# Optimization experiments

Measured on AMD Instinct MI355X. Metric: run time of the kernel, lower is better.

The kernel has to match this reference:

```python
import jax, jax.numpy as jnp
import numpy as np

B, T, D = 16, 2048, 512
DB, K, TOPK, WIN = 128, 7, 16, 64
GATE_CAP = 0.5
STRAND_CAP = 0.5
_PHI = 1.618033988749895
_PSI = -0.6180339887498949


def _ln(x, w, b):
    mu = jnp.mean(x, -1, keepdims=True)
    var = jnp.var(x, -1, keepdims=True)
    return (x - mu) * jax.lax.rsqrt(var + 1e-5) * w + b


def setup_inputs() -> dict:
    key = jax.random.key(0)
    ks = jax.random.split(key, 20)
    def nrm(i, shape, scale=1.0):
        return jax.random.normal(ks[i], shape, dtype=jnp.float32) * jnp.float32(scale)
    return {
        'X_write': nrm(0, (B, T, D)),
        'X_read': nrm(1, (B, T, D)),
        'slots': nrm(2, (B, K, DB)),
        'W0': nrm(3, (D, D), D ** -0.5),
        'ln_write_w': jnp.ones((D,), jnp.float32),
        'ln_write_b': jnp.zeros((D,), jnp.float32),
        'W_V': nrm(4, (D, DB), D ** -0.5),
        'W_K_slot': nrm(5, (DB, DB), DB ** -0.5),
        'slot_key_bias': nrm(6, (K, DB), 2.0),
        'W_gate_w': nrm(7, (2 * DB, DB), (2 * DB) ** -0.5),
        'W_gate_b': jnp.full((DB,), -2.0, jnp.float32),
        'ln_strand_w': jnp.ones((DB,), jnp.float32),
        'ln_strand_b': jnp.zeros((DB,), jnp.float32),
        'Ws_Q': nrm(8, (DB, DB), DB ** -0.5),
        'Ws_K': nrm(9, (DB, DB), DB ** -0.5),
        'Ws_V': nrm(10, (DB, DB), DB ** -0.5),
        'lambda_strand': nrm(11, (DB,), 0.5),
        'W_Q_read': nrm(12, (D, DB), D ** -0.5),
        'W_K_read': nrm(13, (DB, DB), DB ** -0.5),
        'W_V_read': nrm(14, (DB, D), DB ** -0.5),
        'render_coeffs': nrm(15, (K, 3, D), 0.2),
        'slot_temps': jnp.ones((K,), jnp.float32),
    }


def _forward(X_write, X_read, slots, W0, ln_write_w, ln_write_b, W_V, W_K_slot,
             slot_key_bias, W_gate_w, W_gate_b, ln_strand_w, ln_strand_b,
             Ws_Q, Ws_K, Ws_V, lambda_strand, W_Q_read, W_K_read, W_V_read,
             render_coeffs, slot_temps):
    scale = jnp.float32(DB ** -0.5)
    W0_sg = jax.lax.stop_gradient(W0)
    X_n = _ln(X_write, ln_write_w, ln_write_b)

    # ---- windowed salience + topk pair selection (no-grad in original) ----
    X_nsg = jax.lax.stop_gradient(X_n)
    X_W0 = X_nsg @ W0_sg.T                      # [B,T,D]
    NEG = jnp.float32(-1e30)
    sal = []
    for o in range(1, WIN + 1):                 # offset j = i - o, fixed small loop
        s = jnp.sum(X_nsg[:, o:, :] * X_W0[:, :-o, :], axis=-1)  # [B, T-o]
        sal.append(jnp.pad(s, ((0, 0), (o, 0)), constant_values=NEG))
    sal = jnp.stack(sal, axis=-1).reshape(B, T * WIN)
    _, flat_idx = jax.lax.top_k(sal, TOPK)      # [B, TOPK]
    i_idx = flat_idx // WIN
    j_idx = i_idx - (flat_idx % WIN + 1)

    # ---- gather pairs, salience-weighted relation vector ----
    x_newer = jnp.take_along_axis(X_n, i_idx[:, :, None], axis=1)   # [B,TOPK,D]
    x_older = jnp.take_along_axis(X_n, j_idx[:, :, None], axis=1)
    pair_sal = jnp.sum(x_newer * (x_older @ W0_sg.T), axis=-1)      # [B,TOPK]
    alpha = jax.nn.softmax(pair_sal, axis=-1)
    rel = (x_newer - x_older) @ W_V                                 # [B,TOPK,DB]
    R_t = jnp.einsum('bk,bkd->bd', alpha, rel)                      # [B,DB]

    # ---- gated slot write ----
    slot_keys = slots @ W_K_slot + slot_key_bias                    # [B,K,DB]
    compat = jnp.einsum('bkd,bd->bk', slot_keys, R_t) * scale * jax.nn.softplus(slot_temps)
    sw = jax.nn.softmax(compat, axis=-1)
    weighted_R = sw[:, :, None] * R_t[:, None, :]                   # [B,K,DB]
    g = jax.nn.sigmoid(jnp.concatenate([slots, weighted_R], -1) @ W_gate_w + W_gate_b)
    slots_upd = (1.0 - g) * slots + g * weighted_R

    # ---- K x K strand mixer ----
    Bn = _ln(slots_upd, ln_strand_w, ln_strand_b)
    sa = jax.nn.softmax(jnp.einsum('bqd,bkd->bqk', Bn @ Ws_Q, Bn @ Ws_K) * scale, axis=-1)
    ctx = sa @ (Bn @ Ws_V)
    slots_next = slots_upd + ctx * jnp.clip(jnp.tanh(lambda_strand), -STRAND_CAP, STRAND_CAP)

    # ---- aux losses ----
    L_persist = jnp.mean((slots_next - slots) ** 2)
    nrm = jnp.maximum(jnp.linalg.norm(slots_next, axis=-1, keepdims=True), 1e-12)
    Bnorm = slots_next / nrm
    cos = jnp.einsum('bkd,bjd->bkj', Bnorm, Bnorm)
    off = ~jnp.eye(K, dtype=bool)
    L_div = jnp.mean((cos ** 2)[:, off])

    # ---- directional gated read attention ----
    q_r = X_read @ W_Q_read                                         # [B,T,DB]
    k_r = slots_next @ W_K_read                                     # [B,K,DB]
    v_r = slots_next @ W_V_read                                     # [B,K,D]
    scores = jnp.einsum('btd,bkd->btk', q_r, k_r) * scale
    q_mean = jnp.mean(X_read, axis=1)                               # [B,D]
    w0q = q_mean @ W0_sg.T
    denom = jnp.float32(_PHI - _PSI)
    phi_q = (w0q - _PSI * q_mean) / denom
    psi_q = (_PHI * q_mean - w0q) / denom
    phi_mag = jnp.linalg.norm(phi_q, axis=-1, keepdims=True)
    psi_mag = jnp.linalg.norm(psi_q, axis=-1, keepdims=True)
    total = phi_mag + psi_mag + 1e-6
    basis = jnp.concatenate([jnp.ones_like(phi_mag), phi_mag / total, psi_mag / total], -1)  # [B,3]
    gate = jnp.clip(jnp.tanh(jnp.einsum('bi,kid->bkd', basis, render_coeffs)), -GATE_CAP, GATE_CAP)
    z = jnp.einsum('btk,bkd->btd', jax.nn.softmax(scores, axis=-1), v_r * gate)
    return z, slots_next, L_persist, L_div


def reference(X_write, X_read, slots, W0, ln_write_w, ln_write_b, W_V, W_K_slot,
              slot_key_bias, W_gate_w, W_gate_b, ln_strand_w, ln_strand_b,
              Ws_Q, Ws_K, Ws_V, lambda_strand, W_Q_read, W_K_read, W_V_read,
              render_coeffs, slot_temps):
    return _forward(X_write, X_read, slots, W0, ln_write_w, ln_write_b, W_V, W_K_slot,
                    slot_key_bias, W_gate_w, W_gate_b, ln_strand_w, ln_strand_b,
                    Ws_Q, Ws_K, Ws_V, lambda_strand, W_Q_read, W_K_read, W_V_read,
                    render_coeffs, slot_temps)
```

## Files before the change

kernel.cpp:

```cpp
#include <hip/hip_runtime.h>
#include <math.h>

#define B_ 16
#define T_ 2048
#define D_ 512
#define DB_ 128
#define K_ 7
#define TOPK_ 16
#define WIN_ 64

static constexpr float SCALE_ = 0.08838834764831845f;
static constexpr float PHI_ = 1.618033988749895f;
static constexpr float PSI_ = -0.6180339887498949f;
static constexpr float INV_DENOM_ = 0.4472135954999579f;
static constexpr float NEGV = -1e30f;
static constexpr float NEGINF = -3.402823466e38f;
#define IMAXI 0x7FFFFFFF

typedef __attribute__((ext_vector_type(8))) __bf16 bf16x8;
typedef __attribute__((ext_vector_type(8))) unsigned short u16x8;
typedef __attribute__((ext_vector_type(4))) float f32x4;

__device__ inline float softplusf(float x){
    return fmaxf(x, 0.f) + log1pf(expf(-fabsf(x)));
// ... 99 lines not shown
        qpart[((size_t)b_*32 + c)*D_ + tid] = s0;
        qpart[((size_t)b_*32 + c)*D_ + tid + 256] = s1;
    }
}

__global__ __launch_bounds__(256) void gemm_xw0_mfma(const unsigned short* __restrict__ Ah,
                                                     const unsigned short* __restrict__ Al,
                                                     const unsigned short* __restrict__ Wh,
                                                     const unsigned short* __restrict__ Wl,
                                                     float* __restrict__ Cf)
{
    __shared__ __align__(16) unsigned short sAh[2*128*32], sAl[2*128*32], sBh[2*128*32], sBl[2*128*32];
    int t0 = blockIdx.x * 128, d0 = blockIdx.y * 128;
    int tid = threadIdx.x;
    int lane = tid & 63, wid = tid >> 6;
    int wr = wid >> 1, wc = wid & 1;
    int fr = lane & 15;
    int kc2 = ((((lane >> 4) + (fr >> 1)) & 3) * 8);

    f32x4 acc[4][4];
    #pragma unroll
    for (int m = 0; m < 4; m++)
        #pragma unroll
        for (int n = 0; n < 4; n++) acc[m][n] = (f32x4){0.f,0.f,0.f,0.f};

    const unsigned short* gs = (wid==0) ? Ah : (wid==1) ? Al : (wid==2) ? Wh : Wl;
    unsigned short* lsA = (wid==0) ? sAh : (wid==1) ? sAl : (wid==2) ? sBh : sBl;
    int rowoff = (wid < 2) ? t0 : d0;
    int cch = ((lane & 3) - ((lane >> 3) & 3)) & 3;
    const unsigned short* gbase = gs + (size_t)(rowoff + (lane >> 2))*512 + cch*8;

    #pragma unroll
    for (int i = 0; i < 8; i++)
        gload16(gbase + (size_t)(16*i)*512 + 0, lsA + i*512);

    for (int t = 0; t < 16; t++) {
        int cur = t & 1;
        __syncthreads();
        if (t < 15) {
            unsigned short* ls = lsA + (cur^1)*(128*32);
            int kk = (t+1)*32;
            #pragma unroll
            for (int i = 0; i < 8; i++)
                gload16(gbase + (size_t)(16*i)*512 + kk, ls + i*512);
        }
        int bo = cur*(128*32);
        bf16x8 ahf[4], alf[4], bhf[4], blf[4];
        #pragma unroll
        for (int m = 0; m < 4; m++) {
            int r = bo + (wr*64 + m*16 + fr)*32 + kc2;
            ahf[m] = ld_bf8(&sAh[r]);
            alf[m] = ld_bf8(&sAl[r]);
        }
        #pragma unroll
        for (int n = 0; n < 4; n++) {
            int r = bo + (wc*64 + n*16 + fr)*32 + kc2;
            bhf[n] = ld_bf8(&sBh[r]);
            blf[n] = ld_bf8(&sBl[r]);
        }
        #pragma unroll
        for (int m = 0; m < 4; m++)
            #pragma unroll
            for (int n = 0; n < 4; n++) {
                acc[m][n] = __builtin_amdgcn_mfma_f32_16x16x32_bf16(bhf[n], ahf[m], acc[m][n], 0, 0, 0);
                acc[m][n] = __builtin_amdgcn_mfma_f32_16x16x32_bf16(bhf[n], alf[m], acc[m][n], 0, 0, 0);
                acc[m][n] = __builtin_amdgcn_mfma_f32_16x16x32_bf16(blf[n], ahf[m], acc[m][n], 0, 0, 0);
            }
    }

    #pragma unroll
    for (int m = 0; m < 4; m++) {
        int t = t0 + wr*64 + m*16 + fr;
        #pragma unroll
        for (int n = 0; n < 4; n++) {
            int dbase = d0 + wc*64 + n*16 + (lane >> 4)*4;
            *(f32x4*)&Cf[(size_t)t*512 + dbase] = acc[m][n];
        }
    }
}

__global__ __launch_bounds__(256) void sal_mfma(const unsigned short* __restrict__ Xh,
                                                const unsigned short* __restrict__ Xl,
                                                const float* __restrict__ Cf,
                                                float* __restrict__ sal)
{
    int b = blockIdx.x, i0 = blockIdx.y * 64;
    __shared__ __align__(16) unsigned short sAh[64*32], sAl[64*32], sBh[128*32], sBl[128*32];
    int tid = threadIdx.x;
    int lane = tid & 63, wcw = tid >> 6;
    int fr = lane & 15;
    int kc2 = ((((lane >> 4) + (fr >> 1)) & 3) * 8);

    const unsigned short* XhB = Xh + (size_t)b*T_*D_;
    const unsigned short* XlB = Xl + (size_t)b*T_*D_;
    const float* CfB = Cf + (size_t)b*T_*D_;

    f32x4 acc[4][2];
    #pragma unroll
    for (int m = 0; m < 4; m++) { acc[m][0] = (f32x4){0.f,0.f,0.f,0.f}; acc[m][1] = (f32x4){0.f,0.f,0.f,0.f}; }

    int ar = tid >> 2, ac = tid & 3;
    int aslot = (ac + (ar >> 1)) & 3;
    int brow = tid >> 1, bhh = tid & 1;
    int jrow = i0 - 64 + brow;

    uint4 rAh, rAl;
    float4 rB0[2], rB1[2];

    auto LOAD = [&](int kk){
        rAh = *(const uint4*)(XhB + (size_t)(i0 + ar)*512 + kk + ac*8);
        rAl = *(const uint4*)(XlB + (size_t)(i0 + ar)*512 + kk + ac*8);
        #pragma unroll
        for (int cc = 0; cc < 2; cc++) {
            int c = 2*bhh + cc;
            if (jrow >= 0) {
                const float* src = CfB + (size_t)jrow*512 + kk + c*8;
                rB0[cc] = *(const float4*)src;
                rB1[cc] = *(const float4*)(src + 4);
            } else {
                rB0[cc] = make_float4(0.f,0.f,0.f,0.f);
                rB1[cc] = make_float4(0.f,0.f,0.f,0.f);
            }
        }
    };
    auto WRITE = [&](){
        *(uint4*)&sAh[ar*32 + aslot*8] = rAh;
        *(uint4*)&sAl[ar*32 + aslot*8] = rAl;
        #pragma unroll
        for (int cc = 0; cc < 2; cc++) {
            int c = 2*bhh + cc;
            int slot = (c + (brow >> 1)) & 3;
            uint4 hv, lv;
            float4 v0 = rB0[cc], v1 = rB1[cc];
            unsigned int h01 = pkbf(v0.x, v0.y), h23 = pkbf(v0.z, v0.w);
            unsigned int h45 = pkbf(v1.x, v1.y), h67 = pkbf(v1.z, v1.w);
            float r0 = v0.x - __uint_as_float(h01 << 16);
            float r1 = v0.y - __uint_as_float(h01 & 0xFFFF0000u);
            float r2 = v0.z - __uint_as_float(h23 << 16);
            float r3 = v0.w - __uint_as_float(h23 & 0xFFFF0000u);
            float r4 = v1.x - __uint_as_float(h45 << 16);
            float r5 = v1.y - __uint_as_float(h45 & 0xFFFF0000u);
            float r6 = v1.z - __uint_as_float(h67 << 16);
            float r7 = v1.w - __uint_as_float(h67 & 0xFFFF0000u);
            hv.x = h01; hv.y = h23; hv.z = h45; hv.w = h67;
            lv.x = pkbf(r0, r1); lv.y = pkbf(r2, r3); lv.z = pkbf(r4, r5); lv.w = pkbf(r6, r7);
            *(uint4*)&sBh[brow*32 + slot*8] = hv;
            *(uint4*)&sBl[brow*32 + slot*8] = lv;
        }
    };

    LOAD(0);
    for (int t = 0; t < 16; t++) {
        WRITE();
        __syncthreads();
        int kkn = (t+1)*32;
        bf16x8 ahf[4], alf[4], bhf[2], blf[2];
        #pragma unroll
        for (int m = 0; m < 4; m++) {
            int r = (m*16 + fr)*32 + kc2;
            ahf[m] = ld_bf8(&sAh[r]);
            alf[m] = ld_bf8(&sAl[r]);
        }
        #pragma unroll
        for (int n = 0; n < 2; n++) {
            int r = (wcw*32 + n*16 + fr)*32 + kc2;
            bhf[n] = ld_bf8(&sBh[r]);
            blf[n] = ld_bf8(&sBl[r]);
        }
        if (t < 15) LOAD(kkn);
        #pragma unroll
        for (int m = 0; m < 4; m++)
            #pragma unroll
            for (int n = 0; n < 2; n++) {
                acc[m][n] = __builtin_amdgcn_mfma_f32_16x16x32_bf16(ahf[m], bhf[n], acc[m][n], 0, 0, 0);
                acc[m][n] = __builtin_amdgcn_mfma_f32_16x16x32_bf16(ahf[m], blf[n], acc[m][n], 0, 0, 0);
                acc[m][n] = __builtin_amdgcn_mfma_f32_16x16x32_bf16(alf[m], bhf[n], acc[m][n], 0, 0, 0);
            }
        __syncthreads();
    }

    float* salB = sal + (size_t)b*T_*WIN_;
    #pragma unroll
    for (int m = 0; m < 4; m++) {
        #pragma unroll
        for (int n = 0; n < 2; n++) {
            int jl = wcw*32 + n*16 + fr;
            #pragma unroll
            for (int r = 0; r < 4; r++) {
                int il = m*16 + (lane >> 4)*4 + r;
                int o = il - jl + 64;
                if (o >= 1 && o <= 64) {
                    int jg = i0 - 64 + jl;
                    salB[(size_t)(i0 + il)*WIN_ + (o - 1)] = (jg >= 0) ? acc[m][n][r] : NEGV;
                }
            }
        }
    }
}

__global__ __launch_bounds__(256) void topk_stage1(const float* __restrict__ sal,
                                                   float* __restrict__ cv, int* __restrict__ ci,
                                                   const float* __restrict__ qpart,
                                                   const float* __restrict__ W0,
                                                   float* __restrict__ w0p)
{
    int b = blockIdx.x, tid = threadIdx.x;
    if (blockIdx.y >= 64) {
        int c = blockIdx.y - 64;
        __shared__ float qm[D_];
        for (int p = tid; p < D_; p += 256) {
            float s = 0.f;
            for (int cc = 0; cc < 32; cc++) s += qpart[((size_t)b*32 + cc)*D_ + p];
            qm[p] = s * (1.f/2048.f);
        }
        __syncthreads();
        int w = tid >> 6, lane = tid & 63;
        float ph = 0.f, ps = 0.f;
        for (int r = 0; r < 16; r++) {
            int d = c*64 + w*16 + r;
            const float* wr = W0 + (size_t)d*D_;
            float s = 0.f;
            #pragma unroll
            for (int q = 0; q < 8; q++) s += qm[lane + q*64] * wr[lane + q*64];
            #pragma unroll
            for (int off = 32; off; off >>= 1) s += __shfl_xor(s, off);
            float phi = (s - PSI_*qm[d]) * INV_DENOM_;
            float psi = (PHI_*qm[d] - s) * INV_DENOM_;
            ph += phi*phi; ps += psi*psi;
        }
        __shared__ float shp[4], shs[4];
        if (lane == 0) { shp[w] = ph; shs[w] = ps; }
        __syncthreads();
        if (tid == 0) {
            w0p[((size_t)b*8 + c)*2 + 0] = shp[0]+shp[1]+shp[2]+shp[3];
            w0p[((size_t)b*8 + c)*2 + 1] = shs[0]+shs[1]+shs[2]+shs[3];
        }
        return;
    }
    int c = blockIdx.y;
    const float* s = sal + (size_t)b*(T_*WIN_) + (size_t)c*2048;
    int base = c*2048;
    int lane = tid & 63, wvi = tid >> 6;
    float v0=NEGINF,v1=NEGINF,v2=NEGINF,v3=NEGINF,v4=NEGINF,v5=NEGINF,v6=NEGINF,v7=NEGINF;
    int   i0=IMAXI, i1=IMAXI, i2=IMAXI, i3=IMAXI, i4=IMAXI, i5=IMAXI, i6=IMAXI, i7=IMAXI;
    #pragma unroll
    for (int r = 0; r < 8; r++) {
        int p = tid + r*256;
        float v = s[p];
        int idx = base + p;
        if (v > v7 || (v == v7 && idx < i7)) {
            bool b6 = (v > v6) || (v == v6 && idx < i6);
            bool b5 = (v > v5) || (v == v5 && idx < i5);
            bool b4 = (v > v4) || (v == v4 && idx < i4);
            bool b3 = (v > v3) || (v == v3 && idx < i3);
            bool b2 = (v > v2) || (v == v2 && idx < i2);
            bool b1 = (v > v1) || (v == v1 && idx < i1);
            bool b0 = (v > v0) || (v == v0 && idx < i0);
            float n7 = b6 ? v6 : v;             int m7 = b6 ? i6 : idx;
            float n6 = b6 ? (b5 ? v5 : v) : v6; int m6 = b6 ? (b5 ? i5 : idx) : i6;
            float n5 = b5 ? (b4 ? v4 : v) : v5; int m5 = b5 ? (b4 ? i4 : idx) : i5;
            float n4 = b4 ? (b3 ? v3 : v) : v4; int m4 = b4 ? (b3 ? i3 : idx) : i4;
            float n3 = b3 ? (b2 ? v2 : v) : v3; int m3 = b3 ? (b2 ? i2 : idx) : i3;
            float n2 = b2 ? (b1 ? v1 : v) : v2; int m2 = b2 ? (b1 ? i1 : idx) : i2;
            float n1 = b1 ? (b0 ? v0 : v) : v1; int m1 = b1 ? (b0 ? i0 : idx) : i1;
            float n0 = b0 ? v : v0;             int m0 = b0 ? idx : i0;
            v7=n7;i7=m7; v6=n6;i6=m6; v5=n5;i5=m5; v4=n4;i4=m4;
            v3=n3;i3=m3; v2=n2;i2=m2; v1=n1;i1=m1; v0=n0;i0=m0;
        }
    }
    float* cvo = cv + (((size_t)b*64 + c)*64) + wvi*16;
    int*   cio = ci + (((size_t)b*64 + c)*64) + wvi*16;
    for (int r = 0; r < 16; r++) {
        float bv = v0; int bi = i0;
        float wv_ = bv; int wi = bi;
        #pragma unroll
        for (int off = 1; off < 64; off <<= 1) {
            float vx = __shfl_xor(wv_, off);
            int   ix = __shfl_xor(wi, off);
            if (vx > wv_ || (vx == wv_ && ix < wi)) { wv_ = vx; wi = ix; }
        }
        if (bv == wv_ && bi == wi) {
            v0=v1;i0=i1; v1=v2;i1=i2; v2=v3;i2=i3; v3=v4;i3=i4;
            v4=v5;i4=i5; v5=v6;i5=i6; v6=v7;i6=i7; v7=NEGINF;i7=IMAXI;
        }
        if (lane == 0) { cvo[r] = wv_; cio[r] = wi; }
    }
}

__global__ __launch_bounds__(512) void slot_head(
    const unsigned short* __restrict__ Xh, const unsigned short* __restrict__ Xl,
    const float* __restrict__ cv, const int* __restrict__ ci,
    float* __restrict__ yws)
{
    int b = blockIdx.x, tid = threadIdx.x;
    int lane = tid & 63, wvi = tid >> 6;
    __shared__ float scv[128]; __shared__ int sci[128];
    __shared__ float tvv[16]; __shared__ int tii[16];
    __shared__ float alpha[16]; __shared__ int tis[16], tjs[16];

    const float* cvb = cv + (size_t)b*4096;
    const int*   cib = ci + (size_t)b*4096;
    float v0=NEGINF,v1=NEGINF,v2=NEGINF,v3=NEGINF,v4=NEGINF,v5=NEGINF,v6=NEGINF,v7=NEGINF;
    int   i0=IMAXI, i1=IMAXI, i2=IMAXI, i3=IMAXI, i4=IMAXI, i5=IMAXI, i6=IMAXI, i7=IMAXI;
    #pragma unroll
    for (int r = 0; r < 8; r++) {
        int p = tid + r*512;
        float v = cvb[p];
        int idx = cib[p];
        if (v > v7 || (v == v7 && idx < i7)) {
            bool b6 = (v > v6) || (v == v6 && idx < i6);
            bool b5 = (v > v5) || (v == v5 && idx < i5);
            bool b4 = (v > v4) || (v == v4 && idx < i4);
            bool b3 = (v > v3) || (v == v3 && idx < i3);
            bool b2 = (v > v2) || (v == v2 && idx < i2);
            bool b1 = (v > v1) || (v == v1 && idx < i1);
            bool b0 = (v > v0) || (v == v0 && idx < i0);
            float n7 = b6 ? v6 : v;             int m7 = b6 ? i6 : idx;
            float n6 = b6 ? (b5 ? v5 : v) : v6; int m6 = b6 ? (b5 ? i5 : idx) : i6;
            float n5 = b5 ? (b4 ? v4 : v) : v5; int m5 = b5 ? (b4 ? i4 : idx) : i5;
            float n4 = b4 ? (b3 ? v3 : v) : v4; int m4 = b4 ? (b3 ? i3 : idx) : i4;
            float n3 = b3 ? (b2 ? v2 : v) : v3; int m3 = b3 ? (b2 ? i2 : idx) : i3;
            float n2 = b2 ? (b1 ? v1 : v) : v2; int m2 = b2 ? (b1 ? i1 : idx) : i2;
            float n1 = b1 ? (b0 ? v0 : v) : v1; int m1 = b1 ? (b0 ? i0 : idx) : i1;
            float n0 = b0 ? v : v0;             int m0 = b0 ? idx : i0;
            v7=n7;i7=m7; v6=n6;i6=m6; v5=n5;i5=m5; v4=n4;i4=m4;
            v3=n3;i3=m3; v2=n2;i2=m2; v1=n1;i1=m1; v0=n0;i0=m0;
        }
    }
    for (int r = 0; r < 16; r++) {
        float bv = v0; int bi = i0;
        float wv_ = bv; int wi = bi;
        #pragma unroll
        for (int off = 1; off < 64; off <<= 1) {
            float vx = __shfl_xor(wv_, off);
            int   ix = __shfl_xor(wi, off);
            if (vx > wv_ || (vx == wv_ && ix < wi)) { wv_ = vx; wi = ix; }
        }
        if (bv == wv_ && bi == wi) {
            v0=v1;i0=i1; v1=v2;i1=i2; v2=v3;i2=i3; v3=v4;i3=i4;
            v4=v5;i4=i5; v5=v6;i5=i6; v6=v7;i6=i7; v7=NEGINF;i7=IMAXI;
        }
        if (lane == 0) { scv[wvi*16 + r] = wv_; sci[wvi*16 + r] = wi; }
    }
    __syncthreads();
    if (wvi == 0) {
        float a0 = scv[lane], a1 = scv[lane + 64];
        int   e0 = sci[lane], e1 = sci[lane + 64];
        bool sw = (a1 > a0) || (a1 == a0 && e1 < e0);
        float u0 = sw ? a1 : a0; int j0 = sw ? e1 : e0;
        float u1 = sw ? a0 : a1; int j1 = sw ? e0 : e1;
        for (int r = 0; r < 16; r++) {
            float bv = u0; int bi = j0;
            float wv_ = bv; int wi = bi;
            #pragma unroll
            for (int off = 1; off < 64; off <<= 1) {
                float vx = __shfl_xor(wv_, off);
                int   ix = __shfl_xor(wi, off);
                if (vx > wv_ || (vx == wv_ && ix < wi)) { wv_ = vx; wi = ix; }
            }
            if (bv == wv_ && bi == wi) { u0 = u1; j0 = j1; u1 = NEGINF; j1 = IMAXI; }
            if (lane == 0) { tvv[r] = wv_; tii[r] = wi; }
        }
    }
    __syncthreads();
    if (tid < 16) {
        float v = tvv[tid];
        int flat = tii[tid];
        tis[tid] = flat >> 6;
        tjs[tid] = (flat >> 6) - ((flat & 63) + 1);
        float m = v;
        #pragma unroll
        for (int off = 8; off; off >>= 1) m = fmaxf(m, __shfl_xor(m, off, 16));
        float e = expf(v - m);
        float s = e;
        #pragma unroll
        for (int off = 8; off; off >>= 1) s += __shfl_xor(s, off, 16);
        alpha[tid] = e / s;
    }
    __syncthreads();
    {
        float acc = 0.f;
        #pragma unroll
        for (int k = 0; k < 16; k++) {
            int i = tis[k], j = tjs[k];
            float xi = bf2f(Xh[((size_t)b*T_ + i)*D_ + tid]) + bf2f(Xl[((size_t)b*T_ + i)*D_ + tid]);
            float xj = bf2f(Xh[((size_t)b*T_ + j)*D_ + tid]) + bf2f(Xl[((size_t)b*T_ + j)*D_ + tid]);
            acc += alpha[k] * (xi - xj);
        }
        yws[(size_t)b*D_ + tid] = acc;
    }
}

__global__ __launch_bounds__(256) void slot_rt(const float* __restrict__ yws,
                                               const float* __restrict__ W_V,
                                               float* __restrict__ rtp)
{
    int b = blockIdx.x, c = blockIdx.y, tid = threadIdx.x;
    __shared__ float ysl[64];
    __shared__ float hsum[2][DB_];
    if (tid < 64) ysl[tid] = yws[(size_t)b*D_ + c*64 + tid];
    __syncthreads();
    int d = tid & 127, h = tid >> 7;
    float acc = 0.f;
    int e0 = h*32;
    #pragma unroll 8
    for (int e = e0; e < e0 + 32; e++)
        acc += ysl[e] * W_V[(size_t)(c*64 + e)*DB_ + d];
    hsum[h][d] = acc;
    __syncthreads();
    if (tid < DB_) rtp[((size_t)b*8 + c)*DB_ + tid] = hsum[0][tid] + hsum[1][tid];
}

__global__ __launch_bounds__(1024) void slot_main(
    const float* __restrict__ slots_in, const float* __restrict__ rtp,
    const float* __restrict__ W_K_slot, const float* __restrict__ skb,
    const float* __restrict__ Wg, const float* __restrict__ Wgb,
    const float* __restrict__ lnw, const float* __restrict__ lnb,
    const float* __restrict__ WsQ, const float* __restrict__ WsK, const float* __restrict__ WsV,
    const float* __restrict__ lambda_, const float* __restrict__ temps,
    float* __restrict__ snws, float* __restrict__ out_slots,
    float* __restrict__ lpP, float* __restrict__ lpD)
{
    int b = blockIdx.x, tid = threadIdx.x;
    int lane = tid & 63, wvi = tid >> 6;
    __shared__ __align__(16) float wbuf[2*8192];
    __shared__ float Rt[DB_];
    __shared__ float sl[K_][DB_];
    __shared__ float upd[K_][DB_];
    __shared__ float Bn[K_][DB_];
    __shared__ float qq[K_][DB_], kk2[K_][DB_], vv[K_][DB_];
    __shared__ float snsh[K_][DB_];
    __shared__ float pf[1024];
    __shared__ float swv[K_], compat[K_], mu7[K_], rs7[K_], nr7[K_], ldv[K_];
    __shared__ float sa[K_][K_];

    auto ISSUE = [&](const float* src, int buf){
        const float* g = src + (wvi*2)*256 + lane*4;
        float* l = wbuf + buf*8192 + (wvi*2)*256;
        gload16(g, l);
        gload16(g + 256, l + 256);
    };

    int kk_ = tid >> 7, dd_ = tid & 127;
    bool act = tid < K_*DB_;

    ISSUE(W_K_slot, 0);
    for (int p = tid; p < K_*DB_; p += 1024) sl[p>>7][p&127] = slots_in[(size_t)b*K_*DB_ + p];
    if (tid < DB_) {
        float a = 0.f;
        #pragma unroll
        for (int c = 0; c < 8; c++) a += rtp[((size_t)b*8 + c)*DB_ + tid];
        Rt[tid] = a;
    }
    __syncthreads();
    ISSUE(W_K_slot + 8192, 1);
    float kacc = 0.f;
    if (act) {
        #pragma unroll 8
        for (int e = 0; e < 64; e++) kacc += sl[kk_][e] * wbuf[e*DB_ + dd_];
    }
    __syncthreads();
    ISSUE(Wg, 0);
    if (act) {
        #pragma unroll 8
        for (int e = 0; e < 64; e++) kacc += sl[kk_][64+e] * wbuf[8192 + e*DB_ + dd_];
        qq[kk_][dd_] = (kacc + skb[kk_*DB_ + dd_]) * Rt[dd_];
    }
    __syncthreads();
    if (wvi < K_) {
        float acc = qq[wvi][lane] + qq[wvi][lane + 64];
        #pragma unroll
        for (int off = 32; off; off >>= 1) acc += __shfl_xor(acc, off);
        if (lane == 0) compat[wvi] = acc * SCALE_ * softplusf(temps[wvi]);
    }
    __syncthreads();
    if (tid == 0) {
        float m = compat[0];
        for (int k = 1; k < K_; k++) m = fmaxf(m, compat[k]);
        float ssum = 0.f;
        for (int k = 0; k < K_; k++) { float e = expf(compat[k]-m); swv[k] = e; ssum += e; }
        for (int k = 0; k < K_; k++) swv[k] /= ssum;
    }
    __syncthreads();
    ISSUE(Wg + 8192, 1);
    float gacc = 0.f;
    if (act) {
        #pragma unroll 8
        for (int e = 0; e < 64; e++) gacc += sl[kk_][e] * wbuf[e*DB_ + dd_];
    }
    __syncthreads();
    ISSUE(Wg + 16384, 0);
    if (act) {
        #pragma unroll 8
        for (int e = 0; e < 64; e++) gacc += sl[kk_][64+e] * wbuf[8192 + e*DB_ + dd_];
    }
    __syncthreads();
    ISSUE(Wg + 24576, 1);
    float g2acc = 0.f;
    if (act) {
        #pragma unroll 8
        for (int e = 0; e < 64; e++) g2acc += Rt[e] * wbuf[e*DB_ + dd_];
    }
    __syncthreads();
    ISSUE(WsQ, 0);
    if (act) {
        #pragma unroll 8
        for (int e = 0; e < 64; e++) g2acc += Rt[64+e] * wbuf[8192 + e*DB_ + dd_];
        float pre = gacc + swv[kk_]*g2acc + Wgb[dd_];
        float g = 1.f / (1.f + expf(-pre));
        upd[kk_][dd_] = (1.f - g) * sl[kk_][dd_] + g * (swv[kk_] * Rt[dd_]);
    }
    __syncthreads();
    if (wvi < K_) {
        float a0 = upd[wvi][lane], a1 = upd[wvi][lane + 64];
        float s = a0 + a1, ss = a0*a0 + a1*a1;
        #pragma unroll
        for (int off = 32; off; off >>= 1) { s += __shfl_xor(s, off); ss += __shfl_xor(ss, off); }
        if (lane == 0) {
            float mu = s / (float)DB_;
            mu7[wvi] = mu;
            rs7[wvi] = rsqrtf(ss/(float)DB_ - mu*mu + 1e-5f);
        }
    }
    __syncthreads();
    if (act) Bn[kk_][dd_] = (upd[kk_][dd_] - mu7[kk_]) * rs7[kk_] * lnw[dd_] + lnb[dd_];
    __syncthreads();
    ISSUE(WsQ + 8192, 1);
    float qacc = 0.f;
    if (act) {
        #pragma unroll 8
        for (int e = 0; e < 64; e++) qacc += Bn[kk_][e] * wbuf[e*DB_ + dd_];
    }
    __syncthreads();
    ISSUE(WsK, 0);
    if (act) {
        #pragma unroll 8
        for (int e = 0; e < 64; e++) qacc += Bn[kk_][64+e] * wbuf[8192 + e*DB_ + dd_];
// ... 166 lines not shown
    __shared__ float vgs[K_][D_];
    int tid = threadIdx.x;
    for (int p = tid; p < K_*D_; p += 256) {
        kqs[p>>9][p&511] = kq[(size_t)b*K_*D_ + p];
        vgs[p>>9][p&511] = vg[(size_t)b*K_*D_ + p];
    }
    __syncthreads();
    int lane = tid & 63, w = tid >> 6;
    for (int it = 0; it < 16; it++) {
        int t = t0 + w*16 + it;
        const float* x = Xr + ((size_t)b*T_ + t)*D_;
        float xr[8];
        float s[K_] = {0,0,0,0,0,0,0};
        #pragma unroll
        for (int r = 0; r < 8; r++) {
            int e = lane + r*64;
            xr[r] = x[e];
            #pragma unroll
            for (int k = 0; k < K_; k++) s[k] += xr[r] * kqs[k][e];
        }
        #pragma unroll
        for (int k = 0; k < K_; k++)
            for (int off = 32; off; off >>= 1) s[k] += __shfl_xor(s[k], off);
        float sc[K_];
        float m = NEGINF;
        #pragma unroll
        for (int k = 0; k < K_; k++) { sc[k] = s[k] * SCALE_; m = fmaxf(m, sc[k]); }
        float p[K_], ssum = 0.f;
        #pragma unroll
        for (int k = 0; k < K_; k++) { p[k] = expf(sc[k] - m); ssum += p[k]; }
        float inv = 1.f / ssum;
        float* zp = z + ((size_t)b*T_ + t)*D_;
        #pragma unroll
        for (int r = 0; r < 8; r++) {
            int e = lane + r*64;
            float a = 0.f;
            #pragma unroll
            for (int k = 0; k < K_; k++) a += p[k] * vgs[k][e];
            zp[e] = a * inv;
        }
    }
}

extern "C" void kernel_launch(void* const* d_in, const int* in_sizes, int n_in,
                              void* d_out, int out_size, void* d_ws, size_t ws_size,
                              hipStream_t stream)
{
    const float* X_write = (const float*)d_in[0];
    const float* X_read  = (const float*)d_in[1];
    const float* slots   = (const float*)d_in[2];
    const float* W0      = (const float*)d_in[3];
    const float* lnw_w   = (const float*)d_in[4];
    const float* lnw_b   = (const float*)d_in[5];
    const float* W_V     = (const float*)d_in[6];
    const float* W_K_slot= (const float*)d_in[7];
    const float* skb     = (const float*)d_in[8];
    const float* Wg      = (const float*)d_in[9];
    const float* Wgb     = (const float*)d_in[10];
    const float* lns_w   = (const float*)d_in[11];
    const float* lns_b   = (const float*)d_in[12];
    const float* WsQ     = (const float*)d_in[13];
    const float* WsK     = (const float*)d_in[14];
    const float* WsV     = (const float*)d_in[15];
    const float* lambda_ = (const float*)d_in[16];
    const float* WQr     = (const float*)d_in[17];
    const float* WKr     = (const float*)d_in[18];
    const float* WVr     = (const float*)d_in[19];
    const float* rc      = (const float*)d_in[20];
    const float* temps   = (const float*)d_in[21];

    const size_t NXD = (size_t)B_*T_*D_;
    unsigned short* Xh  = (unsigned short*)d_ws;
    unsigned short* Xl  = Xh + NXD;
    float* Cf           = (float*)(Xl + NXD);
    unsigned short* W0h = (unsigned short*)(Cf + NXD);
    unsigned short* W0l = W0h + (size_t)D_*D_;
    float* fscr  = (float*)(W0l + (size_t)D_*D_);
    float* qpart = fscr;
    float* w0p   = qpart + (size_t)B_*32*D_;
    float* snws  = w0p + 256;
    float* kq    = snws + (size_t)B_*K_*DB_;
    float* vg    = kq + (size_t)B_*K_*D_;
    float* cv    = vg + (size_t)B_*K_*D_;
    int*   ci    = (int*)(cv + (size_t)B_*64*64);
    float* lpP   = (float*)(ci + (size_t)B_*64*64);
    float* lpD   = lpP + 16;
    float* yws   = lpD + 16;
    float* rtp   = yws + (size_t)B_*D_;

    float* z_out     = (float*)d_out;
    float* slots_out = z_out + NXD;
    float* loss_out  = slots_out + (size_t)B_*K_*DB_;
    float* sal       = z_out;

    prep_kernel<<<dim3(4096 + 256 + 512), dim3(256), 0, stream>>>(
        X_write, lnw_w, lnw_b, Xh, Xl, W0, W0h, W0l, X_read, qpart);
    gemm_xw0_mfma<<<dim3(B_*T_/128, D_/128), dim3(256), 0, stream>>>(Xh, Xl, W0h, W0l, Cf);
    sal_mfma<<<dim3(B_, T_/64), dim3(256), 0, stream>>>(Xh, Xl, Cf, sal);
    topk_stage1<<<dim3(B_, 72), dim3(256), 0, stream>>>(sal, cv, ci, qpart, W0, w0p);
    slot_head<<<dim3(B_), dim3(512), 0, stream>>>(Xh, Xl, cv, ci, yws);
    slot_rt<<<dim3(B_, 8), dim3(256), 0, stream>>>(yws, W_V, rtp);
    slot_main<<<dim3(B_), dim3(1024), 0, stream>>>(slots, rtp,
        W_K_slot, skb, Wg, Wgb, lns_w, lns_b, WsQ, WsK, WsV, lambda_, temps,
        snws, slots_out, lpP, lpD);
    kqvg_kernel<<<dim3(B_, K_), dim3(256), 0, stream>>>(snws, WKr, WQr, WVr, rc, w0p,
        lpP, lpD, kq, vg, loss_out);
    z_kernel<<<dim3(B_, T_/64), dim3(256), 0, stream>>>(X_read, kq, vg, z_out);
}
```

Baseline: 265.5 us.

## Fuse salience top-k into sal_mfma and merge slot_head/slot_rt into slot_main

The salience tile now stays in shared memory and sal_mfma computes per-row-chunk top-16 candidates directly, so the full salience array is no longer written to global memory and reread by a separate top-k kernel. The final candidate merge, the pair gather and the W_V projection move into slot_main, with W_V streamed through its double buffer, which removes two small launches and their intermediates. The W0·q path becomes its own small kernel. In exchange sal_mfma uses more shared memory (16 KB extra), and the single-block-per-batch slot_main takes on more serial work.

```diff
diff --git a/kernel.cpp b/kernel.cpp
--- a/kernel.cpp
+++ b/kernel.cpp
@@ -205,10 +205,11 @@
 __global__ __launch_bounds__(256) void sal_mfma(const unsigned short* __restrict__ Xh,
                                                 const unsigned short* __restrict__ Xl,
                                                 const float* __restrict__ Cf,
-                                                float* __restrict__ sal)
+                                                float* __restrict__ cv, int* __restrict__ ci)
 {
     int b = blockIdx.x, i0 = blockIdx.y * 64;
     __shared__ __align__(16) unsigned short sAh[64*32], sAl[64*32], sBh[128*32], sBl[128*32];
+    __shared__ float stile[64*64];
     int tid = threadIdx.x;
     int lane = tid & 63, wcw = tid >> 6;
     int fr = lane & 15;
@@ -302,7 +303,6 @@
         __syncthreads();
     }
 
-    float* salB = sal + (size_t)b*T_*WIN_;
     #pragma unroll
     for (int m = 0; m < 4; m++) {
         #pragma unroll
@@ -314,166 +314,47 @@
                 int o = il - jl + 64;
                 if (o >= 1 && o <= 64) {
                     int jg = i0 - 64 + jl;
-                    salB[(size_t)(i0 + il)*WIN_ + (o - 1)] = (jg >= 0) ? acc[m][n][r] : NEGV;
+                    stile[il*64 + (o - 1)] = (jg >= 0) ? acc[m][n][r] : NEGV;
                 }
             }
         }
     }
-}
-
-__global__ __launch_bounds__(256) void topk_stage1(const float* __restrict__ sal,
-                                                   float* __restrict__ cv, int* __restrict__ ci,
-                                                   const float* __restrict__ qpart,
-                                                   const float* __restrict__ W0,
-                                                   float* __restrict__ w0p)
-{
-    int b = blockIdx.x, tid = threadIdx.x;
-    if (blockIdx.y >= 64) {
-        int c = blockIdx.y - 64;
-        __shared__ float qm[D_];
-        for (int p = tid; p < D_; p += 256) {
-            float s = 0.f;
-            for (int cc = 0; cc < 32; cc++) s += qpart[((size_t)b*32 + cc)*D_ + p];
-            qm[p] = s * (1.f/2048.f);
-        }
-        __syncthreads();
-        int w = tid >> 6, lane = tid & 63;
-        float ph = 0.f, ps = 0.f;
+    __syncthreads();
+
+    int wvi = tid >> 6;
+    #pragma unroll
+    for (int h = 0; h < 2; h++) {
+        float v0=NEGINF,v1=NEGINF,v2=NEGINF,v3=NEGINF,v4=NEGINF,v5=NEGINF,v6=NEGINF,v7=NEGINF;
+        int   i0l=IMAXI, i1l=IMAXI, i2l=IMAXI, i3l=IMAXI, i4l=IMAXI, i5l=IMAXI, i6l=IMAXI, i7l=IMAXI;
+        #pragma unroll
+        for (int r = 0; r < 8; r++) {
+            int q = h*2048 + tid + r*256;
+            float v = stile[q];
+            int idx = i0*64 + q;
+            if (v > v7 || (v == v7 && idx < i7l)) {
+                bool b6 = (v > v6) || (v == v6 && idx < i6l);
+                bool b5 = (v > v5) || (v == v5 && idx < i5l);
+                bool b4 = (v > v4) || (v == v4 && idx < i4l);
+                bool b3 = (v > v3) || (v == v3 && idx < i3l);
+                bool b2 = (v > v2) || (v == v2 && idx < i2l);
+                bool b1 = (v > v1) || (v == v1 && idx < i1l);
+                bool b0 = (v > v0) || (v == v0 && idx < i0l);
+                float n7 = b6 ? v6 : v;             int m7 = b6 ? i6l : idx;
+                float n6 = b6 ? (b5 ? v5 : v) : v6; int m6 = b6 ? (b5 ? i5l : idx) : i6l;
+                float n5 = b5 ? (b4 ? v4 : v) : v5; int m5 = b5 ? (b4 ? i4l : idx) : i5l;
+                float n4 = b4 ? (b3 ? v3 : v) : v4; int m4 = b4 ? (b3 ? i3l : idx) : i4l;
+                float n3 = b3 ? (b2 ? v2 : v) : v3; int m3 = b3 ? (b2 ? i2l : idx) : i3l;
+                float n2 = b2 ? (b1 ? v1 : v) : v2; int m2 = b2 ? (b1 ? i1l : idx) : i2l;
+                float n1 = b1 ? (b0 ? v0 : v) : v1; int m1 = b1 ? (b0 ? i0l : idx) : i1l;
+                float n0 = b0 ? v : v0;             int m0 = b0 ? idx : i0l;
+                v7=n7;i7l=m7; v6=n6;i6l=m6; v5=n5;i5l=m5; v4=n4;i4l=m4;
+                v3=n3;i3l=m3; v2=n2;i2l=m2; v1=n1;i1l=m1; v0=n0;i0l=m0;
+            }
+        }
+        float* cvo = cv + (((size_t)b*32 + blockIdx.y)*128) + h*64 + wvi*16;
+        int*   cio = ci + (((size_t)b*32 + blockIdx.y)*128) + h*64 + wvi*16;
         for (int r = 0; r < 16; r++) {
-            int d = c*64 + w*16 + r;
-            const float* wr = W0 + (size_t)d*D_;
-            float s = 0.f;
-            #pragma unroll
-            for (int q = 0; q < 8; q++) s += qm[lane + q*64] * wr[lane + q*64];
-            #pragma unroll
-            for (int off = 32; off; off >>= 1) s += __shfl_xor(s, off);
-            float phi = (s - PSI_*qm[d]) * INV_DENOM_;
-            float psi = (PHI_*qm[d] - s) * INV_DENOM_;
-            ph += phi*phi; ps += psi*psi;
-        }
-        __shared__ float shp[4], shs[4];
-        if (lane == 0) { shp[w] = ph; shs[w] = ps; }
-        __syncthreads();
-        if (tid == 0) {
-            w0p[((size_t)b*8 + c)*2 + 0] = shp[0]+shp[1]+shp[2]+shp[3];
-            w0p[((size_t)b*8 + c)*2 + 1] = shs[0]+shs[1]+shs[2]+shs[3];
-        }
-        return;
-    }
-    int c = blockIdx.y;
-    const float* s = sal + (size_t)b*(T_*WIN_) + (size_t)c*2048;
-    int base = c*2048;
-    int lane = tid & 63, wvi = tid >> 6;
-    float v0=NEGINF,v1=NEGINF,v2=NEGINF,v3=NEGINF,v4=NEGINF,v5=NEGINF,v6=NEGINF,v7=NEGINF;
-    int   i0=IMAXI, i1=IMAXI, i2=IMAXI, i3=IMAXI, i4=IMAXI, i5=IMAXI, i6=IMAXI, i7=IMAXI;
-    #pragma unroll
-    for (int r = 0; r < 8; r++) {
-        int p = tid + r*256;
-        float v = s[p];
-        int idx = base + p;
-        if (v > v7 || (v == v7 && idx < i7)) {
-            bool b6 = (v > v6) || (v == v6 && idx < i6);
-            bool b5 = (v > v5) || (v == v5 && idx < i5);
-            bool b4 = (v > v4) || (v == v4 && idx < i4);
-            bool b3 = (v > v3) || (v == v3 && idx < i3);
-            bool b2 = (v > v2) || (v == v2 && idx < i2);
-            bool b1 = (v > v1) || (v == v1 && idx < i1);
-            bool b0 = (v > v0) || (v == v0 && idx < i0);
-            float n7 = b6 ? v6 : v;             int m7 = b6 ? i6 : idx;
-            float n6 = b6 ? (b5 ? v5 : v) : v6; int m6 = b6 ? (b5 ? i5 : idx) : i6;
-            float n5 = b5 ? (b4 ? v4 : v) : v5; int m5 = b5 ? (b4 ? i4 : idx) : i5;
-            float n4 = b4 ? (b3 ? v3 : v) : v4; int m4 = b4 ? (b3 ? i3 : idx) : i4;
-            float n3 = b3 ? (b2 ? v2 : v) : v3; int m3 = b3 ? (b2 ? i2 : idx) : i3;
-            float n2 = b2 ? (b1 ? v1 : v) : v2; int m2 = b2 ? (b1 ? i1 : idx) : i2;
-            float n1 = b1 ? (b0 ? v0 : v) : v1; int m1 = b1 ? (b0 ? i0 : idx) : i1;
-            float n0 = b0 ? v : v0;             int m0 = b0 ? idx : i0;
-            v7=n7;i7=m7; v6=n6;i6=m6; v5=n5;i5=m5; v4=n4;i4=m4;
-            v3=n3;i3=m3; v2=n2;i2=m2; v1=n1;i1=m1; v0=n0;i0=m0;
-        }
-    }
-    float* cvo = cv + (((size_t)b*64 + c)*64) + wvi*16;
-    int*   cio = ci + (((size_t)b*64 + c)*64) + wvi*16;
-    for (int r = 0; r < 16; r++) {
-        float bv = v0; int bi = i0;
-        float wv_ = bv; int wi = bi;
-        #pragma unroll
-        for (int off = 1; off < 64; off <<= 1) {
-            float vx = __shfl_xor(wv_, off);
-            int   ix = __shfl_xor(wi, off);
-            if (vx > wv_ || (vx == wv_ && ix < wi)) { wv_ = vx; wi = ix; }
-        }
-        if (bv == wv_ && bi == wi) {
-            v0=v1;i0=i1; v1=v2;i1=i2; v2=v3;i2=i3; v3=v4;i3=i4;
-            v4=v5;i4=i5; v5=v6;i5=i6; v6=v7;i6=i7; v7=NEGINF;i7=IMAXI;
-        }
-        if (lane == 0) { cvo[r] = wv_; cio[r] = wi; }
-    }
-}
-
-__global__ __launch_bounds__(512) void slot_head(
-    const unsigned short* __restrict__ Xh, const unsigned short* __restrict__ Xl,
-    const float* __restrict__ cv, const int* __restrict__ ci,
-    float* __restrict__ yws)
-{
-    int b = blockIdx.x, tid = threadIdx.x;
-    int lane = tid & 63, wvi = tid >> 6;
-    __shared__ float scv[128]; __shared__ int sci[128];
-    __shared__ float tvv[16]; __shared__ int tii[16];
-    __shared__ float alpha[16]; __shared__ int tis[16], tjs[16];
-
-    const float* cvb = cv + (size_t)b*4096;
-    const int*   cib = ci + (size_t)b*4096;
-    float v0=NEGINF,v1=NEGINF,v2=NEGINF,v3=NEGINF,v4=NEGINF,v5=NEGINF,v6=NEGINF,v7=NEGINF;
-    int   i0=IMAXI, i1=IMAXI, i2=IMAXI, i3=IMAXI, i4=IMAXI, i5=IMAXI, i6=IMAXI, i7=IMAXI;
-    #pragma unroll
-    for (int r = 0; r < 8; r++) {
-        int p = tid + r*512;
-        float v = cvb[p];
-        int idx = cib[p];
-        if (v > v7 || (v == v7 && idx < i7)) {
-            bool b6 = (v > v6) || (v == v6 && idx < i6);
-            bool b5 = (v > v5) || (v == v5 && idx < i5);
-            bool b4 = (v > v4) || (v == v4 && idx < i4);
-            bool b3 = (v > v3) || (v == v3 && idx < i3);
-            bool b2 = (v > v2) || (v == v2 && idx < i2);
-            bool b1 = (v > v1) || (v == v1 && idx < i1);
-            bool b0 = (v > v0) || (v == v0 && idx < i0);
-            float n7 = b6 ? v6 : v;             int m7 = b6 ? i6 : idx;
-            float n6 = b6 ? (b5 ? v5 : v) : v6; int m6 = b6 ? (b5 ? i5 : idx) : i6;
-            float n5 = b5 ? (b4 ? v4 : v) : v5; int m5 = b5 ? (b4 ? i4 : idx) : i5;
-            float n4 = b4 ? (b3 ? v3 : v) : v4; int m4 = b4 ? (b3 ? i3 : idx) : i4;
-            float n3 = b3 ? (b2 ? v2 : v) : v3; int m3 = b3 ? (b2 ? i2 : idx) : i3;
-            float n2 = b2 ? (b1 ? v1 : v) : v2; int m2 = b2 ? (b1 ? i1 : idx) : i2;
-            float n1 = b1 ? (b0 ? v0 : v) : v1; int m1 = b1 ? (b0 ? i0 : idx) : i1;
-            float n0 = b0 ? v : v0;             int m0 = b0 ? idx : i0;
-            v7=n7;i7=m7; v6=n6;i6=m6; v5=n5;i5=m5; v4=n4;i4=m4;
-            v3=n3;i3=m3; v2=n2;i2=m2; v1=n1;i1=m1; v0=n0;i0=m0;
-        }
-    }
-    for (int r = 0; r < 16; r++) {
-        float bv = v0; int bi = i0;
-        float wv_ = bv; int wi = bi;
-        #pragma unroll
-        for (int off = 1; off < 64; off <<= 1) {
-            float vx = __shfl_xor(wv_, off);
-            int   ix = __shfl_xor(wi, off);
-            if (vx > wv_ || (vx == wv_ && ix < wi)) { wv_ = vx; wi = ix; }
-        }
-        if (bv == wv_ && bi == wi) {
-            v0=v1;i0=i1; v1=v2;i1=i2; v2=v3;i2=i3; v3=v4;i3=i4;
-            v4=v5;i4=i5; v5=v6;i5=i6; v6=v7;i6=i7; v7=NEGINF;i7=IMAXI;
-        }
-        if (lane == 0) { scv[wvi*16 + r] = wv_; sci[wvi*16 + r] = wi; }
-    }
-    __syncthreads();
-    if (wvi == 0) {
-        float a0 = scv[lane], a1 = scv[lane + 64];
-        int   e0 = sci[lane], e1 = sci[lane + 64];
-        bool sw = (a1 > a0) || (a1 == a0 && e1 < e0);
-        float u0 = sw ? a1 : a0; int j0 = sw ? e1 : e0;
-        float u1 = sw ? a0 : a1; int j1 = sw ? e0 : e1;
-        for (int r = 0; r < 16; r++) {
-            float bv = u0; int bi = j0;
+            float bv = v0; int bi = i0l;
             float wv_ = bv; int wi = bi;
             #pragma unroll
             for (int off = 1; off < 64; off <<= 1) {
@@ -481,61 +362,55 @@
                 int   ix = __shfl_xor(wi, off);
                 if (vx > wv_ || (vx == wv_ && ix < wi)) { wv_ = vx; wi = ix; }
             }
-            if (bv == wv_ && bi == wi) { u0 = u1; j0 = j1; u1 = NEGINF; j1 = IMAXI; }
-            if (lane == 0) { tvv[r] = wv_; tii[r] = wi; }
-        }
-    }
-    __syncthreads();
-    if (tid < 16) {
-        float v = tvv[tid];
-        int flat = tii[tid];
-        tis[tid] = flat >> 6;
-        tjs[tid] = (flat >> 6) - ((flat & 63) + 1);
-        float m = v;
-        #pragma unroll
-        for (int off = 8; off; off >>= 1) m = fmaxf(m, __shfl_xor(m, off, 16));
-        float e = expf(v - m);
-        float s = e;
-        #pragma unroll
-        for (int off = 8; off; off >>= 1) s += __shfl_xor(s, off, 16);
-        alpha[tid] = e / s;
-    }
-    __syncthreads();
-    {
-        float acc = 0.f;
-        #pragma unroll
-        for (int k = 0; k < 16; k++) {
-            int i = tis[k], j = tjs[k];
-            float xi = bf2f(Xh[((size_t)b*T_ + i)*D_ + tid]) + bf2f(Xl[((size_t)b*T_ + i)*D_ + tid]);
-            float xj = bf2f(Xh[((size_t)b*T_ + j)*D_ + tid]) + bf2f(Xl[((size_t)b*T_ + j)*D_ + tid]);
-            acc += alpha[k] * (xi - xj);
-        }
-        yws[(size_t)b*D_ + tid] = acc;
-    }
-}
-
-__global__ __launch_bounds__(256) void slot_rt(const float* __restrict__ yws,
-                                               const float* __restrict__ W_V,
-                                               float* __restrict__ rtp)
+            if (bv == wv_ && bi == wi) {
+                v0=v1;i0l=i1l; v1=v2;i1l=i2l; v2=v3;i2l=i3l; v3=v4;i3l=i4l;
+                v4=v5;i4l=i5l; v5=v6;i5l=i6l; v6=v7;i6l=i7l; v7=NEGINF;i7l=IMAXI;
+            }
+            if (lane == 0) { cvo[r] = wv_; cio[r] = wi; }
+        }
+    }
+}
+
+__global__ __launch_bounds__(256) void w0q_kernel(const float* __restrict__ qpart,
+                                                  const float* __restrict__ W0,
+                                                  float* __restrict__ w0p)
 {
     int b = blockIdx.x, c = blockIdx.y, tid = threadIdx.x;
-    __shared__ float ysl[64];
-    __shared__ float hsum[2][DB_];
-    if (tid < 64) ysl[tid] = yws[(size_t)b*D_ + c*64 + tid];
-    __syncthreads();
-    int d = tid & 127, h = tid >> 7;
-    float acc = 0.f;
-    int e0 = h*32;
-    #pragma unroll 8
-    for (int e = e0; e < e0 + 32; e++)
-        acc += ysl[e] * W_V[(size_t)(c*64 + e)*DB_ + d];
-    hsum[h][d] = acc;
-    __syncthreads();
-    if (tid < DB_) rtp[((size_t)b*8 + c)*DB_ + tid] = hsum[0][tid] + hsum[1][tid];
+    __shared__ float qm[D_];
+    for (int p = tid; p < D_; p += 256) {
+        float s = 0.f;
+        for (int cc = 0; cc < 32; cc++) s += qpart[((size_t)b*32 + cc)*D_ + p];
+        qm[p] = s * (1.f/2048.f);
+    }
+    __syncthreads();
+    int w = tid >> 6, lane = tid & 63;
+    float ph = 0.f, ps = 0.f;
+    for (int r = 0; r < 16; r++) {
+        int d = c*64 + w*16 + r;
+        const float* wr = W0 + (size_t)d*D_;
+        float s = 0.f;
+        #pragma unroll
+        for (int q = 0; q < 8; q++) s += qm[lane + q*64] * wr[lane + q*64];
+        #pragma unroll
+        for (int off = 32; off; off >>= 1) s += __shfl_xor(s, off);
+        float phi = (s - PSI_*qm[d]) * INV_DENOM_;
+        float psi = (PHI_*qm[d] - s) * INV_DENOM_;
+        ph += phi*phi; ps += psi*psi;
+    }
+    __shared__ float shp[4], shs[4];
+    if (lane == 0) { shp[w] = ph; shs[w] = ps; }
+    __syncthreads();
+    if (tid == 0) {
+        w0p[((size_t)b*8 + c)*2 + 0] = shp[0]+shp[1]+shp[2]+shp[3];
+        w0p[((size_t)b*8 + c)*2 + 1] = shs[0]+shs[1]+shs[2]+shs[3];
+    }
 }
 
 __global__ __launch_bounds__(1024) void slot_main(
-    const float* __restrict__ slots_in, const float* __restrict__ rtp,
+    const unsigned short* __restrict__ Xh, const unsigned short* __restrict__ Xl,
+    const float* __restrict__ slots_in,
+    const float* __restrict__ cv, const int* __restrict__ ci,
+    const float* __restrict__ W_V,
     const float* __restrict__ W_K_slot, const float* __restrict__ skb,
     const float* __restrict__ Wg, const float* __restrict__ Wgb,
     const float* __restrict__ lnw, const float* __restrict__ lnb,
@@ -547,6 +422,8 @@
     int b = blockIdx.x, tid = threadIdx.x;
     int lane = tid & 63, wvi = tid >> 6;
     __shared__ __align__(16) float wbuf[2*8192];
+    __shared__ float yb[D_];
+    __shared__ float part[8][DB_];
     __shared__ float Rt[DB_];
     __shared__ float sl[K_][DB_];
     __shared__ float upd[K_][DB_];
@@ -554,6 +431,9 @@
     __shared__ float qq[K_][DB_], kk2[K_][DB_], vv[K_][DB_];
     __shared__ float snsh[K_][DB_];
     __shared__ float pf[1024];
+    __shared__ float scv[256]; __shared__ int sci[256];
+    __shared__ float tvv[16]; __shared__ int tii[16];
+    __shared__ float alpha[16]; __shared__ int tis[16], tjs[16];
     __shared__ float swv[K_], compat[K_], mu7[K_], rs7[K_], nr7[K_], ldv[K_];
     __shared__ float sa[K_][K_];
 
@@ -567,15 +447,130 @@
     int kk_ = tid >> 7, dd_ = tid & 127;
     bool act = tid < K_*DB_;
 
-    ISSUE(W_K_slot, 0);
+    ISSUE(W_V, 0);
     for (int p = tid; p < K_*DB_; p += 1024) sl[p>>7][p&127] = slots_in[(size_t)b*K_*DB_ + p];
+
+    {
+        const float* cvb = cv + (size_t)b*4096;
+        const int*   cib = ci + (size_t)b*4096;
+        float v0=NEGINF,v1=NEGINF,v2=NEGINF,v3=NEGINF;
+        int   i0=IMAXI, i1=IMAXI, i2=IMAXI, i3=IMAXI;
+        #pragma unroll
+        for (int r = 0; r < 4; r++) {
+            int p = tid + r*1024;
+            float v = cvb[p];
+            int idx = cib[p];
+            if (v > v3 || (v == v3 && idx < i3)) {
+                bool b2 = (v > v2) || (v == v2 && idx < i2);
+                bool b1 = (v > v1) || (v == v1 && idx < i1);
+                bool b0 = (v > v0) || (v == v0 && idx < i0);
+                float n3 = b2 ? v2 : v;             int m3 = b2 ? i2 : idx;
+                float n2 = b2 ? (b1 ? v1 : v) : v2; int m2 = b2 ? (b1 ? i1 : idx) : i2;
+                float n1 = b1 ? (b0 ? v0 : v) : v1; int m1 = b1 ? (b0 ? i0 : idx) : i1;
+                float n0 = b0 ? v : v0;             int m0 = b0 ? idx : i0;
+                v3=n3;i3=m3; v2=n2;i2=m2; v1=n1;i1=m1; v0=n0;i0=m0;
+            }
+        }
+        for (int r = 0; r < 16; r++) {
+            float bv = v0; int bi = i0;
+            float wv_ = bv; int wi = bi;
+            #pragma unroll
+            for (int off = 1; off < 64; off <<= 1) {
+                float vx = __shfl_xor(wv_, off);
+                int   ix = __shfl_xor(wi, off);
+                if (vx > wv_ || (vx == wv_ && ix < wi)) { wv_ = vx; wi = ix; }
+            }
+            if (bv == wv_ && bi == wi) {
+                v0=v1;i0=i1; v1=v2;i1=i2; v2=v3;i2=i3; v3=NEGINF;i3=IMAXI;
+            }
+            if (lane == 0) { scv[wvi*16 + r] = wv_; sci[wvi*16 + r] = wi; }
+        }
+        __syncthreads();
+        if (wvi == 0) {
+            float u0=NEGINF,u1=NEGINF,u2=NEGINF,u3=NEGINF;
+            int   j0=IMAXI, j1=IMAXI, j2=IMAXI, j3=IMAXI;
+            #pragma unroll
+            for (int r = 0; r < 4; r++) {
+                int p = lane + r*64;
+                float v = scv[p]; int idx = sci[p];
+                if (v > u3 || (v == u3 && idx < j3)) {
+                    bool b2 = (v > u2) || (v == u2 && idx < j2);
+                    bool b1 = (v > u1) || (v == u1 && idx < j1);
+                    bool b0 = (v > u0) || (v == u0 && idx < j0);
+                    float n3 = b2 ? u2 : v;             int m3 = b2 ? j2 : idx;
+                    float n2 = b2 ? (b1 ? u1 : v) : u2; int m2 = b2 ? (b1 ? j1 : idx) : j2;
+                    float n1 = b1 ? (b0 ? u0 : v) : u1; int m1 = b1 ? (b0 ? j0 : idx) : j1;
+                    float n0 = b0 ? v : u0;             int m0 = b0 ? idx : j0;
+                    u3=n3;j3=m3; u2=n2;j2=m2; u1=n1;j1=m1; u0=n0;j0=m0;
+                }
+            }
+            for (int r = 0; r < 16; r++) {
+                float bv = u0; int bi = j0;
+                float wv_ = bv; int wi = bi;
+                #pragma unroll
+                for (int off = 1; off < 64; off <<= 1) {
+                    float vx = __shfl_xor(wv_, off);
+                    int   ix = __shfl_xor(wi, off);
+                    if (vx > wv_ || (vx == wv_ && ix < wi)) { wv_ = vx; wi = ix; }
+                }
+                if (bv == wv_ && bi == wi) {
+                    u0=u1;j0=j1; u1=u2;j1=j2; u2=u3;j2=j3; u3=NEGINF;j3=IMAXI;
+                }
+                if (lane == 0) { tvv[r] = wv_; tii[r] = wi; }
+            }
+        }
+        __syncthreads();
+    }
+    if (tid < 16) {
+        float v = tvv[tid];
+        int flat = tii[tid];
+        tis[tid] = flat >> 6;
+        tjs[tid] = (flat >> 6) - ((flat & 63) + 1);
+        float m = v;
+        #pragma unroll
+        for (int off = 8; off; off >>= 1) m = fmaxf(m, __shfl_xor(m, off, 16));
+        float e = expf(v - m);
+        float s = e;
+        #pragma unroll
+        for (int off = 8; off; off >>= 1) s += __shfl_xor(s, off, 16);
+        alpha[tid] = e / s;
+    }
+    __syncthreads();
+    if (tid < D_) {
+        float acc = 0.f;
+        #pragma unroll
+        for (int k = 0; k < 16; k++) {
+            int i = tis[k], j = tjs[k];
+            float xi = bf2f(Xh[((size_t)b*T_ + i)*D_ + tid]) + bf2f(Xl[((size_t)b*T_ + i)*D_ + tid]);
+            float xj = bf2f(Xh[((size_t)b*T_ + j)*D_ + tid]) + bf2f(Xl[((size_t)b*T_ + j)*D_ + tid]);
+            acc += alpha[k] * (xi - xj);
+        }
+        yb[tid] = acc;
+    }
+    __syncthreads();
+
+    int gg = tid >> 7;
+    float rtacc = 0.f;
+    #pragma unroll
+    for (int c = 0; c < 8; c++) {
+        if (c < 7) ISSUE(W_V + (size_t)(c+1)*8192, (c+1)&1);
+        else ISSUE(W_K_slot, 0);
+        int p = (c&1)*8192;
+        #pragma unroll
+        for (int e = 0; e < 8; e++)
+            rtacc += yb[c*64 + gg*8 + e] * wbuf[p + (gg*8+e)*DB_ + dd_];
+        __syncthreads();
+    }
+    part[gg][dd_] = rtacc;
+    __syncthreads();
     if (tid < DB_) {
         float a = 0.f;
         #pragma unroll
-        for (int c = 0; c < 8; c++) a += rtp[((size_t)b*8 + c)*DB_ + tid];
+        for (int g = 0; g < 8; g++) a += part[g][tid];
         Rt[tid] = a;
     }
     __syncthreads();
+
     ISSUE(W_K_slot + 8192, 1);
     float kacc = 0.f;
     if (act) {
@@ -908,25 +903,20 @@
     float* kq    = snws + (size_t)B_*K_*DB_;
     float* vg    = kq + (size_t)B_*K_*D_;
     float* cv    = vg + (size_t)B_*K_*D_;
-    int*   ci    = (int*)(cv + (size_t)B_*64*64);
-    float* lpP   = (float*)(ci + (size_t)B_*64*64);
+    int*   ci    = (int*)(cv + (size_t)B_*4096);
+    float* lpP   = (float*)(ci + (size_t)B_*4096);
     float* lpD   = lpP + 16;
-    float* yws   = lpD + 16;
-    float* rtp   = yws + (size_t)B_*D_;
 
     float* z_out     = (float*)d_out;
     float* slots_out = z_out + NXD;
     float* loss_out  = slots_out + (size_t)B_*K_*DB_;
-    float* sal       = z_out;
 
     prep_kernel<<<dim3(4096 + 256 + 512), dim3(256), 0, stream>>>(
         X_write, lnw_w, lnw_b, Xh, Xl, W0, W0h, W0l, X_read, qpart);
     gemm_xw0_mfma<<<dim3(B_*T_/128, D_/128), dim3(256), 0, stream>>>(Xh, Xl, W0h, W0l, Cf);
-    sal_mfma<<<dim3(B_, T_/64), dim3(256), 0, stream>>>(Xh, Xl, Cf, sal);
-    topk_stage1<<<dim3(B_, 72), dim3(256), 0, stream>>>(sal, cv, ci, qpart, W0, w0p);
-    slot_head<<<dim3(B_), dim3(512), 0, stream>>>(Xh, Xl, cv, ci, yws);
-    slot_rt<<<dim3(B_, 8), dim3(256), 0, stream>>>(yws, W_V, rtp);
-    slot_main<<<dim3(B_), dim3(1024), 0, stream>>>(slots, rtp,
+    sal_mfma<<<dim3(B_, T_/64), dim3(256), 0, stream>>>(Xh, Xl, Cf, cv, ci);
+    w0q_kernel<<<dim3(B_, 8), dim3(256), 0, stream>>>(qpart, W0, w0p);
+    slot_main<<<dim3(B_), dim3(1024), 0, stream>>>(Xh, Xl, slots, cv, ci, W_V,
         W_K_slot, skb, Wg, Wgb, lns_w, lns_b, WsQ, WsK, WsV, lambda_, temps,
         snws, slots_out, lpP, lpD);
     kqvg_kernel<<<dim3(B_, K_), dim3(256), 0, stream>>>(snws, WKr, WQr, WVr, rc, w0p,
```

After: 276.0 us. 1.04x slower.
